# Kernel tuning notes

Hardware: AMD Instinct MI355X
Metric: run time of the kernel (lower is better)

## Reference

```python
import jax, jax.numpy as jnp
import numpy as np

N_DEV, N_CAT, N_APP = 100, 1000, 100000
D = 256
E = 100000

EDGES = [("dev", "app", "ei_dev_app", "ew_dev_app"),
         ("app", "cat", "ei_app_cat", "ew_app_cat"),
         ("app", "app", "ei_app_app", "ew_app_app")]
SIZES = {"dev": N_DEV, "cat": N_CAT, "app": N_APP}


def setup_inputs() -> dict:
    key = jax.random.key(0)
    ks = jax.random.split(key, 32)
    s = 1.0 / np.sqrt(D)
    inp = {
        "x_dev": jax.random.normal(ks[0], (N_DEV, D), jnp.float32),
        "x_cat": jax.random.normal(ks[1], (N_CAT, D), jnp.float32),
        "x_app": jax.random.normal(ks[2], (N_APP, D), jnp.float32),
        "ei_dev_app": jnp.stack([jax.random.randint(ks[3], (E,), 0, N_DEV),
                                 jax.random.randint(ks[4], (E,), 0, N_APP)]).astype(jnp.int32),
        "ei_app_cat": jnp.stack([jax.random.randint(ks[5], (E,), 0, N_APP),
                                 jax.random.randint(ks[6], (E,), 0, N_CAT)]).astype(jnp.int32),
        "ei_app_app": jnp.stack([jax.random.randint(ks[7], (E,), 0, N_APP),
                                 jax.random.randint(ks[8], (E,), 0, N_APP)]).astype(jnp.int32),
        "ew_dev_app": jax.random.uniform(ks[9], (E,), jnp.float32, 0.5, 2.0),
        "ew_app_cat": jax.random.uniform(ks[10], (E,), jnp.float32, 0.5, 2.0),
        "ew_app_app": jax.random.uniform(ks[11], (E,), jnp.float32, 0.5, 2.0),
    }
    # per-node-type linear params for layer1 and layer2 (torch nn.Linear equivalents)
    i = 12
    for layer in (1, 2):
        for t in ("dev", "cat", "app"):
            inp[f"W{layer}_{t}"] = jax.random.normal(ks[i], (D, D), jnp.float32) * s
            inp[f"b{layer}_{t}"] = jax.random.normal(ks[i + 1], (D,), jnp.float32) * s
            i += 2
    return inp


def _mp_layer(x, params, ei, ew):
    """One MyMessagePassing layer: per-src-type linear+relu, edge-weighted
    gather, scatter-add into destination node type."""
    # src-type transform (same math as doing it per edge-type iteration)
    h = {t: jax.nn.relu(x[t] @ params[t][0] + params[t][1]) for t in x}
    out = {t: jnp.zeros((SIZES[t], D), x[t].dtype) for t in x}
    for src, dst, ei_name, ew_name in EDGES:
        idx = ei[ei_name]
        msg = h[src][idx[0]] * ew[ew_name][:, None]  # [E, D]
        out[dst] = out[dst] + jax.ops.segment_sum(msg, idx[1], num_segments=SIZES[dst])
    return out


def reference(x_dev, x_cat, x_app,
              ei_dev_app, ei_app_cat, ei_app_app,
              ew_dev_app, ew_app_cat, ew_app_app,
              W1_dev, b1_dev, W1_cat, b1_cat, W1_app, b1_app,
              W2_dev, b2_dev, W2_cat, b2_cat, W2_app, b2_app):
    ei = {"ei_dev_app": ei_dev_app, "ei_app_cat": ei_app_cat, "ei_app_app": ei_app_app}
    ew = {"ew_dev_app": ew_dev_app, "ew_app_cat": ew_app_cat, "ew_app_app": ew_app_app}
    x = {"dev": x_dev, "cat": x_cat, "app": x_app}
    p1 = {"dev": (W1_dev, b1_dev), "cat": (W1_cat, b1_cat), "app": (W1_app, b1_app)}
    p2 = {"dev": (W2_dev, b2_dev), "cat": (W2_cat, b2_cat), "app": (W2_app, b2_app)}
    x = _mp_layer(x, p1, ei, ew)
    x = _mp_layer(x, p2, ei, ew)
    return (x["dev"], x["cat"], x["app"])
```

## Files before the change

kernel.cpp:

```cpp
#include <hip/hip_runtime.h>
#include <cstdint>
#include <cstddef>

#define DD 256
constexpr int NDEV = 100;
constexpr int NCAT = 1000;
constexpr int NAPP = 100000;
constexpr int NE   = 100000;
constexpr int NCNT = NAPP + NAPP + NCAT;

__global__ __launch_bounds__(256)
void linear_relu_kernel(const float* __restrict__ A, const float* __restrict__ W,
                        const float* __restrict__ bias, float* __restrict__ C,
                        int M) {
    __shared__ float As[8][128];
    __shared__ float Bs[8][128];

    const int t  = threadIdx.x;
    const int m0 = blockIdx.x * 128;
    const int n0 = blockIdx.y * 128;
    const int ra = (t >> 4) << 2;
    const int ca = (t & 15) << 2;

    float acc[8][8];
#pragma unroll
    for (int i = 0; i < 8; ++i)
#pragma unroll
        for (int j = 0; j < 8; ++j) acc[i][j] = 0.f;

    for (int k0 = 0; k0 < DD; k0 += 8) {
        {
            const int row = t >> 1;
            const int kk  = (t & 1) << 2;
            float4 v = make_float4(0.f, 0.f, 0.f, 0.f);
            if (m0 + row < M)
                v = *(const float4*)(A + (size_t)(m0 + row) * DD + k0 + kk);
            As[kk + 0][row] = v.x;
            As[kk + 1][row] = v.y;
            As[kk + 2][row] = v.z;
            As[kk + 3][row] = v.w;
        }
        {
            const int kk = t >> 5;
            const int nn = (t & 31) << 2;
            *(float4*)&Bs[kk][nn] =
                *(const float4*)(W + (size_t)(k0 + kk) * DD + n0 + nn);
        }
        __syncthreads();
#pragma unroll
        for (int k = 0; k < 8; ++k) {
            const float4 a0 = *(const float4*)&As[k][ra];
            const float4 a1 = *(const float4*)&As[k][ra + 64];
            const float4 b0 = *(const float4*)&Bs[k][ca];
            const float4 b1 = *(const float4*)&Bs[k][ca + 64];
            const float av[8] = {a0.x, a0.y, a0.z, a0.w, a1.x, a1.y, a1.z, a1.w};
            const float bv[8] = {b0.x, b0.y, b0.z, b0.w, b1.x, b1.y, b1.z, b1.w};
#pragma unroll
            for (int i = 0; i < 8; ++i)
#pragma unroll
                for (int j = 0; j < 8; ++j)
                    acc[i][j] = fmaf(av[i], bv[j], acc[i][j]);
        }
        __syncthreads();
    }

    const float4 bias0 = *(const float4*)(bias + n0 + ca);
    const float4 bias1 = *(const float4*)(bias + n0 + ca + 64);
#pragma unroll
    for (int i = 0; i < 8; ++i) {
        const int row = m0 + ((i < 4) ? (ra + i) : (ra + 64 + i - 4));
        if (row >= M) continue;
        float4 o0, o1;
        o0.x = fmaxf(acc[i][0] + bias0.x, 0.f);
        o0.y = fmaxf(acc[i][1] + bias0.y, 0.f);
        o0.z = fmaxf(acc[i][2] + bias0.z, 0.f);
        o0.w = fmaxf(acc[i][3] + bias0.w, 0.f);
        o1.x = fmaxf(acc[i][4] + bias1.x, 0.f);
        o1.y = fmaxf(acc[i][5] + bias1.y, 0.f);
        o1.z = fmaxf(acc[i][6] + bias1.z, 0.f);
        o1.w = fmaxf(acc[i][7] + bias1.w, 0.f);
        *(float4*)(C + (size_t)row * DD + n0 + ca)      = o0;
        *(float4*)(C + (size_t)row * DD + n0 + ca + 64) = o1;
    }
}

__global__ __launch_bounds__(256)
void hist3_kernel(const int* __restrict__ d_aa, const int* __restrict__ d_da,
                  const int* __restrict__ d_ac, int* __restrict__ counts) {
    const int g = blockIdx.x * 256 + threadIdx.x;
    if (g < NE)            atomicAdd(&counts[d_aa[g]], 1);
    else if (g < 2 * NE)   atomicAdd(&counts[NAPP + d_da[g - NE]], 1);
    else if (g < 3 * NE)   atomicAdd(&counts[2 * NAPP + d_ac[g - 2 * NE]], 1);
}

__global__ __launch_bounds__(256)
void scan_partial_kernel(const int* __restrict__ counts, int* __restrict__ bsum,
                         int n) {
    __shared__ int sd[256];
    const int t   = threadIdx.x;
    const int idx = blockIdx.x * 1024 + t * 4;
    int s = 0;
    if (idx + 3 < n) {
        const int4 c = *(const int4*)(counts + idx);
        s = c.x + c.y + c.z + c.w;
    } else {
        for (int j = 0; j < 4; ++j) if (idx + j < n) s += counts[idx + j];
    }
    sd[t] = s;
    __syncthreads();
    for (int off = 128; off > 0; off >>= 1) {
        if (t < off) sd[t] += sd[t + off];
        __syncthreads();
    }
    if (t == 0) bsum[blockIdx.x] = sd[0];
}

__global__ __launch_bounds__(256)
void scan_bsum_kernel(const int* __restrict__ bsum, int* __restrict__ boff, int nb) {
    __shared__ int sd[256];
    const int t = threadIdx.x;
    const int v = (t < nb) ? bsum[t] : 0;
    sd[t] = v;
    __syncthreads();
    for (int off = 1; off < 256; off <<= 1) {
        const int w = (t >= off) ? sd[t - off] : 0;
        __syncthreads();
        sd[t] += w;
        __syncthreads();
    }
    if (t < nb) boff[t] = sd[t] - v;
}

__global__ __launch_bounds__(256)
void scan_apply_kernel(int* __restrict__ counts, const int* __restrict__ boff,
                       int* __restrict__ rs, int n) {
    __shared__ int sd[256];
    const int t   = threadIdx.x;
    const int idx = blockIdx.x * 1024 + t * 4;
    int c[4] = {0, 0, 0, 0};
    if (idx + 3 < n) {
        const int4 v = *(const int4*)(counts + idx);
        c[0] = v.x; c[1] = v.y; c[2] = v.z; c[3] = v.w;
    } else {
        for (int j = 0; j < 4; ++j) if (idx + j < n) c[j] = counts[idx + j];
    }
    const int s = c[0] + c[1] + c[2] + c[3];
    sd[t] = s;
    __syncthreads();
    for (int off = 1; off < 256; off <<= 1) {
        const int w = (t >= off) ? sd[t - off] : 0;
        __syncthreads();
        sd[t] += w;
        __syncthreads();
    }
    int o = boff[blockIdx.x] + sd[t] - s;
#pragma unroll
    for (int j = 0; j < 4; ++j) {
        const int i = idx + j;
        if (i < n) {
            rs[i]     = o;
            counts[i] = o;
            o += c[j];
            if (i == n - 1) rs[n] = o;
        }
    }
}

__global__ __launch_bounds__(256)
void fill3_kernel(const int* __restrict__ ei_aa, const float* __restrict__ ew_aa,
                  const int* __restrict__ ei_da, const float* __restrict__ ew_da,
                  const int* __restrict__ ei_ac, const float* __restrict__ ew_ac,
                  int* __restrict__ cursor, int* __restrict__ srcs,
                  float* __restrict__ wsorted) {
    const int g = blockIdx.x * 256 + threadIdx.x;
    if (g >= 3 * NE) return;
    const int*   ei;
    const float* ew;
    int e, base;
    if (g < NE)            { ei = ei_aa; ew = ew_aa; e = g;          base = 0; }
    else if (g < 2 * NE)   { ei = ei_da; ew = ew_da; e = g - NE;     base = NAPP; }
    else                   { ei = ei_ac; ew = ew_ac; e = g - 2 * NE; base = 2 * NAPP; }
    const int d   = ei[NE + e];
    const int pos = atomicAdd(&cursor[base + d], 1);
    srcs[pos]    = ei[e];
    wsorted[pos] = ew[e];
}

__global__ __launch_bounds__(256)
void gather_l1_app_kernel(const float* __restrict__ hA, const float* __restrict__ hD,
                          const int* __restrict__ rsA, const int* __restrict__ rsD,
                          const int* __restrict__ s, const float* __restrict__ w,
                          float* __restrict__ out, int ndst) {
    const int d    = (int)((blockIdx.x * 256 + threadIdx.x) >> 6);
    const int lane = threadIdx.x & 63;
    if (d >= ndst) return;
    const int o = lane << 2;
    float4 acc = make_float4(0.f, 0.f, 0.f, 0.f);
    for (int p = rsA[d], pe = rsA[d + 1]; p < pe; ++p) {
        const float  ww = w[p];
        const float4 v  = *(const float4*)(hA + (size_t)s[p] * DD + o);
        acc.x = fmaf(ww, v.x, acc.x);
        acc.y = fmaf(ww, v.y, acc.y);
        acc.z = fmaf(ww, v.z, acc.z);
        acc.w = fmaf(ww, v.w, acc.w);
    }
    for (int p = rsD[d], pe = rsD[d + 1]; p < pe; ++p) {
        const float  ww = w[p];
        const float4 v  = *(const float4*)(hD + (size_t)s[p] * DD + o);
        acc.x = fmaf(ww, v.x, acc.x);
        acc.y = fmaf(ww, v.y, acc.y);
        acc.z = fmaf(ww, v.z, acc.z);
        acc.w = fmaf(ww, v.w, acc.w);
    }
    *(float4*)(out + (size_t)d * DD + o) = acc;
}

__global__ __launch_bounds__(256)
void gather_l2_app_kernel(const float* __restrict__ hA,
                          const int* __restrict__ rsA, const int* __restrict__ rsD,
                          const int* __restrict__ s, const float* __restrict__ w,
                          const float* __restrict__ b2dev,
                          float* __restrict__ out, int ndst) {
    const int d    = (int)((blockIdx.x * 256 + threadIdx.x) >> 6);
    const int lane = threadIdx.x & 63;
    if (d >= ndst) return;
    const int o = lane << 2;
    float4 acc = make_float4(0.f, 0.f, 0.f, 0.f);
    for (int p = rsA[d], pe = rsA[d + 1]; p < pe; ++p) {
        const float  ww = w[p];
        const float4 v  = *(const float4*)(hA + (size_t)s[p] * DD + o);
        acc.x = fmaf(ww, v.x, acc.x);
        acc.y = fmaf(ww, v.y, acc.y);
        acc.z = fmaf(ww, v.z, acc.z);
        acc.w = fmaf(ww, v.w, acc.w);
    }
    float wsum = 0.f;
    for (int p = rsD[d], pe = rsD[d + 1]; p < pe; ++p) wsum += w[p];
    const float4 b = *(const float4*)(b2dev + o);
    acc.x = fmaf(wsum, fmaxf(b.x, 0.f), acc.x);
    acc.y = fmaf(wsum, fmaxf(b.y, 0.f), acc.y);
    acc.z = fmaf(wsum, fmaxf(b.z, 0.f), acc.z);
    acc.w = fmaf(wsum, fmaxf(b.w, 0.f), acc.w);
    *(float4*)(out + (size_t)d * DD + o) = acc;
}

__global__ __launch_bounds__(256)
void gather_cat_kernel(const float* __restrict__ hA,
                       const int* __restrict__ rs, const int* __restrict__ s,
                       const float* __restrict__ w,
                       float* __restrict__ out, int ndst) {
    const int d    = (int)((blockIdx.x * 256 + threadIdx.x) >> 6);
    const int lane = threadIdx.x & 63;
    if (d >= ndst) return;
    const int o = lane << 2;
    float4 acc = make_float4(0.f, 0.f, 0.f, 0.f);
    for (int p = rs[d], pe = rs[d + 1]; p < pe; ++p) {
        const float  ww = w[p];
        const float4 v  = *(const float4*)(hA + (size_t)s[p] * DD + o);
        acc.x = fmaf(ww, v.x, acc.x);
        acc.y = fmaf(ww, v.y, acc.y);
        acc.z = fmaf(ww, v.z, acc.z);
        acc.w = fmaf(ww, v.w, acc.w);
    }
    *(float4*)(out + (size_t)d * DD + o) = acc;
}

extern "C" void kernel_launch(void* const* d_in, const int* in_sizes, int n_in,
                              void* d_out, int out_size, void* d_ws, size_t ws_size,
                              hipStream_t stream) {
    const float* x_dev  = (const float*)d_in[0];
    const float* x_app  = (const float*)d_in[2];
    const int*   ei_da  = (const int*)d_in[3];
    const int*   ei_ac  = (const int*)d_in[4];
    const int*   ei_aa  = (const int*)d_in[5];
    const float* ew_da  = (const float*)d_in[6];
    const float* ew_ac  = (const float*)d_in[7];
    const float* ew_aa  = (const float*)d_in[8];
    const float* W1_dev = (const float*)d_in[9];
    const float* b1_dev = (const float*)d_in[10];
    const float* W1_app = (const float*)d_in[13];
    const float* b1_app = (const float*)d_in[14];
    const float* b2_dev = (const float*)d_in[16];
    const float* W2_app = (const float*)d_in[19];
    const float* b2_app = (const float*)d_in[20];

    float* out     = (float*)d_out;
    float* out_cat = out + (size_t)NDEV * DD;
    float* out_app = out + (size_t)(NDEV + NCAT) * DD;

    float* h_app  = (float*)d_ws;
    float* h_dev  = h_app + (size_t)NAPP * DD;
    int*   counts = (int*)(h_dev + (size_t)NDEV * DD);
    int*   rs_all = counts + NCNT;
    int*   s_all  = rs_all + NCNT + 1;
    float* w_all  = (float*)(s_all + 3 * NE);
    int*   bsum   = (int*)(w_all + 3 * NE);
    int*   boff   = bsum + 256;

    int* rs_aa = rs_all;
    int* rs_da = rs_all + NAPP;
    int* rs_ac = rs_all + 2 * NAPP;

    const int  nblk = (NCNT + 1023) / 1024;
    const dim3 gApp((NAPP + 127) / 128, 2);
    const int  gGatherApp = (NAPP + 3) / 4;
    const int  gGatherCat = (NCAT + 3) / 4;
    const int  g3e = (3 * NE + 255) / 256;

    hipMemsetAsync(counts, 0, (size_t)NCNT * sizeof(int), stream);
    hist3_kernel<<<g3e, 256, 0, stream>>>(ei_aa + NE, ei_da + NE, ei_ac + NE, counts);
    scan_partial_kernel<<<nblk, 256, 0, stream>>>(counts, bsum, NCNT);
    scan_bsum_kernel<<<1, 256, 0, stream>>>(bsum, boff, nblk);
    scan_apply_kernel<<<nblk, 256, 0, stream>>>(counts, boff, rs_all, NCNT);
    fill3_kernel<<<g3e, 256, 0, stream>>>(ei_aa, ew_aa, ei_da, ew_da, ei_ac, ew_ac,
                                          counts, s_all, w_all);

    linear_relu_kernel<<<gApp, 256, 0, stream>>>(x_app, W1_app, b1_app, h_app, NAPP);
    linear_relu_kernel<<<dim3(1, 2), 256, 0, stream>>>(x_dev, W1_dev, b1_dev, h_dev, NDEV);
    gather_l1_app_kernel<<<gGatherApp, 256, 0, stream>>>(
        h_app, h_dev, rs_aa, rs_da, s_all, w_all, out_app, NAPP);

    linear_relu_kernel<<<gApp, 256, 0, stream>>>(out_app, W2_app, b2_app, h_app, NAPP);
    gather_l2_app_kernel<<<gGatherApp, 256, 0, stream>>>(
        h_app, rs_aa, rs_da, s_all, w_all, b2_dev, out_app, NAPP);
    gather_cat_kernel<<<gGatherCat, 256, 0, stream>>>(
        h_app, rs_ac, s_all, w_all, out_cat, NCAT);

    hipMemsetAsync(out, 0, (size_t)NDEV * DD * sizeof(float), stream);
}
```

Baseline: 780.8 us.

## Use split-bf16 MFMA for the large app-node linear+ReLU GEMMs

Replaces the fp32 SIMT tiled GEMM for the 100k-row app linear layers with a matrix-core kernel. Each fp32 operand is split into bf16 hi and lo parts, and hi*hi + lo*hi + hi*lo products are accumulated in fp32 to stay close to fp32 accuracy. Weights are pre-split and transposed by a small extra kernel into a workspace region that reuses the histogram counts buffer, which is no longer needed at that point. The aim is to cut GEMM compute time, at the cost of three MFMA passes per tile, conversion overhead when staging A, and a small loss of precision.

```diff
diff --git a/kernel.cpp b/kernel.cpp
--- a/kernel.cpp
+++ b/kernel.cpp
@@ -8,6 +8,150 @@
 constexpr int NAPP = 100000;
 constexpr int NE   = 100000;
 constexpr int NCNT = NAPP + NAPP + NCAT;
+
+typedef __attribute__((ext_vector_type(8))) short  bf16x8;
+typedef __attribute__((ext_vector_type(8))) unsigned short ushort8;
+typedef __attribute__((ext_vector_type(4))) float  f32x4;
+
+__device__ __forceinline__ unsigned short f2bf(float f) {
+    unsigned int u = __float_as_uint(f);
+    u += 0x7fffu + ((u >> 16) & 1u);
+    return (unsigned short)(u >> 16);
+}
+__device__ __forceinline__ float bf2f(unsigned short h) {
+    return __uint_as_float((unsigned int)h << 16);
+}
+
+__global__ __launch_bounds__(256)
+void wsplit_kernel(const float* __restrict__ W, unsigned short* __restrict__ hi,
+                   unsigned short* __restrict__ lo) {
+    const int idx = blockIdx.x * 256 + threadIdx.x;
+    const int k = idx >> 8, n = idx & 255;
+    const float f = W[idx];
+    const unsigned short h = f2bf(f);
+    hi[n * 256 + k] = h;
+    lo[n * 256 + k] = f2bf(f - bf2f(h));
+}
+
+#define BK 32
+#define PAD 40
+
+__global__ __launch_bounds__(256, 2)
+void linear_relu_mfma_kernel(const float* __restrict__ A,
+                             const unsigned short* __restrict__ Wt_hi,
+                             const unsigned short* __restrict__ Wt_lo,
+                             const float* __restrict__ bias,
+                             float* __restrict__ C, int M) {
+    __shared__ unsigned short As_hi[128][PAD];
+    __shared__ unsigned short As_lo[128][PAD];
+    __shared__ unsigned short Ws_hi[256][PAD];
+    __shared__ unsigned short Ws_lo[256][PAD];
+
+    const int t    = threadIdx.x;
+    const int wave = t >> 6;
+    const int lane = t & 63;
+    const int cl   = lane & 15;
+    const int kg8  = (lane >> 4) * 8;
+    const int m0   = blockIdx.x * 128;
+    const int n0w  = wave * 64;
+
+    f32x4 acc[8][4];
+#pragma unroll
+    for (int m = 0; m < 8; ++m)
+#pragma unroll
+        for (int n = 0; n < 4; ++n) acc[m][n] = (f32x4){0.f, 0.f, 0.f, 0.f};
+
+    const int ar = t >> 1;
+    const int ak = (t & 1) * 16;
+
+    for (int k0 = 0; k0 < DD; k0 += BK) {
+        {
+            float fv[16];
+            if (m0 + ar < M) {
+                const float* p = A + (size_t)(m0 + ar) * DD + k0 + ak;
+#pragma unroll
+                for (int i = 0; i < 4; ++i) {
+                    const float4 v = *(const float4*)(p + i * 4);
+                    fv[i * 4 + 0] = v.x; fv[i * 4 + 1] = v.y;
+                    fv[i * 4 + 2] = v.z; fv[i * 4 + 3] = v.w;
+                }
+            } else {
+#pragma unroll
+                for (int i = 0; i < 16; ++i) fv[i] = 0.f;
+            }
+#pragma unroll
+            for (int g = 0; g < 2; ++g) {
+                ushort8 hh, ll;
+#pragma unroll
+                for (int j = 0; j < 8; ++j) {
+                    const float f = fv[g * 8 + j];
+                    const unsigned short h = f2bf(f);
+                    hh[j] = h;
+                    ll[j] = f2bf(f - bf2f(h));
+                }
+                *(ushort8*)&As_hi[ar][ak + g * 8] = hh;
+                *(ushort8*)&As_lo[ar][ak + g * 8] = ll;
+            }
+        }
+        {
+            const unsigned short* ph = Wt_hi + (size_t)t * DD + k0;
+            const unsigned short* pl = Wt_lo + (size_t)t * DD + k0;
+#pragma unroll
+            for (int g = 0; g < 4; ++g) {
+                *(ushort8*)&Ws_hi[t][g * 8] = *(const ushort8*)(ph + g * 8);
+                *(ushort8*)&Ws_lo[t][g * 8] = *(const ushort8*)(pl + g * 8);
+            }
+        }
+        __syncthreads();
+
+        bf16x8 ah[8], al[8], bb[4];
+#pragma unroll
+        for (int m = 0; m < 8; ++m) {
+            ah[m] = *(const bf16x8*)&As_hi[m * 16 + cl][kg8];
+            al[m] = *(const bf16x8*)&As_lo[m * 16 + cl][kg8];
+        }
+#pragma unroll
+        for (int n = 0; n < 4; ++n)
+            bb[n] = *(const bf16x8*)&Ws_hi[n0w + n * 16 + cl][kg8];
+#pragma unroll
+        for (int m = 0; m < 8; ++m)
+#pragma unroll
+            for (int n = 0; n < 4; ++n)
+                acc[m][n] = __builtin_amdgcn_mfma_f32_16x16x32_bf16(
+                    ah[m], bb[n], acc[m][n], 0, 0, 0);
+#pragma unroll
+        for (int m = 0; m < 8; ++m)
+#pragma unroll
+            for (int n = 0; n < 4; ++n)
+                acc[m][n] = __builtin_amdgcn_mfma_f32_16x16x32_bf16(
+                    al[m], bb[n], acc[m][n], 0, 0, 0);
+#pragma unroll
+        for (int n = 0; n < 4; ++n)
+            bb[n] = *(const bf16x8*)&Ws_lo[n0w + n * 16 + cl][kg8];
+#pragma unroll
+        for (int m = 0; m < 8; ++m)
+#pragma unroll
+            for (int n = 0; n < 4; ++n)
+                acc[m][n] = __builtin_amdgcn_mfma_f32_16x16x32_bf16(
+                    ah[m], bb[n], acc[m][n], 0, 0, 0);
+        __syncthreads();
+    }
+
+    const int r4 = (lane >> 4) << 2;
+#pragma unroll
+    for (int n = 0; n < 4; ++n) {
+        const int col = n0w + n * 16 + cl;
+        const float bv = bias[col];
+#pragma unroll
+        for (int m = 0; m < 8; ++m) {
+            const int rowb = m0 + m * 16 + r4;
+            float* cp = C + (size_t)rowb * DD + col;
+#pragma unroll
+            for (int j = 0; j < 4; ++j)
+                if (rowb + j < M) cp[(size_t)j * DD] = fmaxf(acc[m][n][j] + bv, 0.f);
+        }
+    }
+}
 
 __global__ __launch_bounds__(256)
 void linear_relu_kernel(const float* __restrict__ A, const float* __restrict__ W,
@@ -301,8 +445,13 @@
     int* rs_da = rs_all + NAPP;
     int* rs_ac = rs_all + 2 * NAPP;
 
+    unsigned short* wt1_hi = (unsigned short*)counts;
+    unsigned short* wt1_lo = wt1_hi + 65536;
+    unsigned short* wt2_hi = wt1_lo + 65536;
+    unsigned short* wt2_lo = wt2_hi + 65536;
+
     const int  nblk = (NCNT + 1023) / 1024;
-    const dim3 gApp((NAPP + 127) / 128, 2);
+    const int  gMfma = (NAPP + 127) / 128;
     const int  gGatherApp = (NAPP + 3) / 4;
     const int  gGatherCat = (NCAT + 3) / 4;
     const int  g3e = (3 * NE + 255) / 256;
@@ -315,12 +464,18 @@
     fill3_kernel<<<g3e, 256, 0, stream>>>(ei_aa, ew_aa, ei_da, ew_da, ei_ac, ew_ac,
                                           counts, s_all, w_all);
 
-    linear_relu_kernel<<<gApp, 256, 0, stream>>>(x_app, W1_app, b1_app, h_app, NAPP);
-    linear_relu_kernel<<<dim3(1, 2), 256, 0, stream>>>(x_dev, W1_dev, b1_dev, h_dev, NDEV);
+    wsplit_kernel<<<256, 256, 0, stream>>>(W1_app, wt1_hi, wt1_lo);
+    wsplit_kernel<<<256, 256, 0, stream>>>(W2_app, wt2_hi, wt2_lo);
+
+    linear_relu_mfma_kernel<<<gMfma, 256, 0, stream>>>(x_app, wt1_hi, wt1_lo,
+                                                       b1_app, h_app, NAPP);
+    linear_relu_kernel<<<dim3(1, 2), 256, 0, stream>>>(x_dev, W1_dev, b1_dev,
+                                                       h_dev, NDEV);
     gather_l1_app_kernel<<<gGatherApp, 256, 0, stream>>>(
         h_app, h_dev, rs_aa, rs_da, s_all, w_all, out_app, NAPP);
 
-    linear_relu_kernel<<<gApp, 256, 0, stream>>>(out_app, W2_app, b2_app, h_app, NAPP);
+    linear_relu_mfma_kernel<<<gMfma, 256, 0, stream>>>(out_app, wt2_hi, wt2_lo,
+                                                       b2_app, h_app, NAPP);
     gather_l2_app_kernel<<<gGatherApp, 256, 0, stream>>>(
         h_app, rs_aa, rs_da, s_all, w_all, b2_dev, out_app, NAPP);
     gather_cat_kernel<<<gGatherCat, 256, 0, stream>>>(
```

After: 641.2 us. 1.22x faster.
